# Optimization experiments

Hardware: AMD Instinct MI355X
Metric: run time of the kernel (lower is better)

## Reference

```python
import jax, jax.numpy as jnp
import numpy as np

D_MODEL = 2048
NUM_HEADS = 16
HEAD_DIM = D_MODEL // NUM_HEADS
BATCH = 2
SEQ = 2048


def setup_inputs() -> dict:
    key = jax.random.key(0)
    ks = jax.random.split(key, 5)
    s = 1.0 / np.sqrt(D_MODEL)
    return {
        "x": jax.random.normal(ks[0], (BATCH, SEQ, D_MODEL), dtype=jnp.float32),
        "Wq": jax.random.normal(ks[1], (D_MODEL, D_MODEL), dtype=jnp.float32) * s,
        "Wk": jax.random.normal(ks[2], (D_MODEL, D_MODEL), dtype=jnp.float32) * s,
        "Wv": jax.random.normal(ks[3], (D_MODEL, D_MODEL), dtype=jnp.float32) * s,
        "Wo": jax.random.normal(ks[4], (D_MODEL, D_MODEL), dtype=jnp.float32) * s,
    }


def reference(x, Wq, Wk, Wv, Wo):
    B, S, D = x.shape
    H, Dh = NUM_HEADS, HEAD_DIM
    # nn.Linear(bias=False): y = x @ W.T ; split_heads is a plain view (no transpose!)
    Q = (x @ Wq.T).reshape(B, H, S, Dh)
    K = (x @ Wk.T).reshape(B, H, S, Dh)
    V = (x @ Wv.T).reshape(B, H, S, Dh)
    # scores scaled by head_dim (NOT sqrt) — faithful to source
    scores = jnp.einsum("bhqd,bhkd->bhqk", Q, K) / jnp.float32(Dh)
    causal_mask = jnp.triu(jnp.ones((S, S), dtype=bool), k=1)  # True above diagonal
    scores = jnp.where(causal_mask, -jnp.inf, scores)
    attn = jax.nn.softmax(scores, axis=-1)
    out = jnp.einsum("bhqk,bhkd->bhqd", attn, V)  # [B,H,S,Dh]
    out = out.transpose(0, 2, 1, 3).reshape(B, S, D)  # merge DOES transpose
    return out @ Wo.T
```

## Files before the change

### kernel.cpp

```cpp
#include <hip/hip_runtime.h>
#include <hip/hip_bf16.h>

using bf16 = __hip_bfloat16;
typedef __attribute__((ext_vector_type(8))) short bf16x8;
typedef __attribute__((ext_vector_type(4))) float f32x4;

#define DEVI __device__ __forceinline__

constexpr int Bn = 2, Sn = 2048, Dn = 2048, Hn = 16, DHn = 128;
constexpr int Mn = Bn * Sn;

DEVI void gload_lds16(const bf16* g, bf16* l) {
  __builtin_amdgcn_global_load_lds(
      (__attribute__((address_space(1))) void*)g,
      (__attribute__((address_space(3))) void*)l,
      16, 0, 0);
}

__global__ __launch_bounds__(256) void cvt_all_k(const float* __restrict__ x,
                                                 const float* __restrict__ wq,
                                                 const float* __restrict__ wk,
                                                 const float* __restrict__ wv,
                                                 const float* __restrict__ wo,
                                                 bf16* __restrict__ xb,
                                                 bf16* __restrict__ wb) {
  const int which = blockIdx.y;
  const float* src;
  bf16* dst;
  int n8;
  if (which == 0) { src = x;  dst = xb; n8 = Mn * Dn / 8; }
  else {
    src = (which == 1) ? wq : (which == 2) ? wk : (which == 3) ? wv : wo;
    dst = wb + (size_t)(which - 1) * Dn * Dn;
    n8 = Dn * Dn / 8;
  }
  for (int i = blockIdx.x * 256 + threadIdx.x; i < n8; i += gridDim.x * 256) {
    const float4* p = (const float4*)src + (size_t)i * 2;
    float4 a = p[0], b = p[1];
    union { bf16 h[8]; bf16x8 v; } u;
    u.h[0] = __float2bfloat16(a.x); u.h[1] = __float2bfloat16(a.y);
    u.h[2] = __float2bfloat16(a.z); u.h[3] = __float2bfloat16(a.w);
    u.h[4] = __float2bfloat16(b.x); u.h[5] = __float2bfloat16(b.y);
    u.h[6] = __float2bfloat16(b.z); u.h[7] = __float2bfloat16(b.w);
    *((bf16x8*)dst + i) = u.v;
  }
}

template <int NTOT, int NMAT>
__global__ __launch_bounds__(256, 2) void gemmY(const bf16* __restrict__ A,
                                                const bf16* __restrict__ W,
                                                bf16* __restrict__ Cv) {
  constexpr int K = 2048, NT = 64;
  __shared__ bf16 smem[2 * 12288];

  const int nwg = NTOT * 16;
  const int orig = blockIdx.x;
  const int wgid = (orig & 7) * (nwg >> 3) + (orig >> 3);
  const int bm = wgid / NTOT;
  const int bnn = wgid % NTOT;
  constexpr int nper = NTOT / NMAT;
  const int z = bnn / nper;
  const int col0 = (bnn % nper) * 128;

  const int t = threadIdx.x;
  const int wave = t >> 6, lane = t & 63;
  const int wm = wave >> 1, wn = wave & 1;
  const int lr = lane & 15, lg = lane >> 4;
  const int rch = ((lg ^ ((lr >> 1) & 3)) * 8);
  const int srow = t >> 2;
  const int sch = (t & 3) ^ ((t >> 3) & 3);

  const bf16* Ab = A + (size_t)(bm * 256 + srow) * K + sch * 8;
  const bf16* Bb = W + (size_t)z * (2048 * 2048) +
                   (size_t)(col0 + srow) * K + sch * 8;

  auto stgA = [&](int slot, int kt, int u) {
    gload_lds16(Ab + (size_t)u * 64 * K + kt * 32,
                smem + slot * 12288 + u * 2048 + t * 8);
  };
  auto stgB = [&](int slot, int kt, int v) {
    gload_lds16(Bb + (size_t)v * 64 * K + kt * 32,
                smem + slot * 12288 + 8192 + v * 2048 + t * 8);
  };

  f32x4 acc[8][4];
  const f32x4 zf = {0.f, 0.f, 0.f, 0.f};
#pragma unroll
  for (int i = 0; i < 8; ++i)
#pragma unroll
    for (int j = 0; j < 4; ++j) acc[i][j] = zf;

  stgA(0, 0, 0); stgA(0, 0, 1); stgA(0, 0, 2); stgA(0, 0, 3);
  stgB(0, 0, 0); stgB(0, 0, 1);
  stgA(1, 1, 0); stgA(1, 1, 2); stgB(1, 1, 0); stgB(1, 1, 1);

#pragma unroll 2
  for (int kt = 0; kt < NT; ++kt) {
    const int slot = kt & 1;
    const bf16* sAb = smem + slot * 12288;
    const bf16* sBb = sAb + 8192;

    if (kt == NT - 1) asm volatile("s_waitcnt vmcnt(0)" ::: "memory");
    else              asm volatile("s_waitcnt vmcnt(4)" ::: "memory");
    __builtin_amdgcn_s_barrier();

    bf16x8 af[4], bv[4];
#pragma unroll
    for (int i = 0; i < 4; ++i)
      af[i] = *(const bf16x8*)(sAb + (wm * 128 + i * 16 + lr) * 32 + rch);
#pragma unroll
    for (int n = 0; n < 4; ++n)
      bv[n] = *(const bf16x8*)(sBb + (wn * 64 + n * 16 + lr) * 32 + rch);
    if (kt + 1 < NT) { stgA(slot ^ 1, kt + 1, 1); stgA(slot ^ 1, kt + 1, 3); }
    asm volatile("s_waitcnt lgkmcnt(0)" ::: "memory");
    __builtin_amdgcn_sched_barrier(0);
    __builtin_amdgcn_s_setprio(1);
#pragma unroll
    for (int i = 0; i < 4; ++i)
#pragma unroll
      for (int n = 0; n < 4; ++n)
        acc[i][n] = __builtin_amdgcn_mfma_f32_16x16x32_bf16(af[i], bv[n], acc[i][n], 0, 0, 0);
    __builtin_amdgcn_s_setprio(0);
    __builtin_amdgcn_s_barrier();

#pragma unroll
    for (int i = 0; i < 4; ++i)
      af[i] = *(const bf16x8*)(sAb + (wm * 128 + 64 + i * 16 + lr) * 32 + rch);
    if (kt + 2 < NT) {
      stgA(slot, kt + 2, 0); stgA(slot, kt + 2, 2);
      stgB(slot, kt + 2, 0); stgB(slot, kt + 2, 1);
    }
    asm volatile("s_waitcnt lgkmcnt(0)" ::: "memory");
    __builtin_amdgcn_sched_barrier(0);
    __builtin_amdgcn_s_setprio(1);
#pragma unroll
    for (int i = 0; i < 4; ++i)
#pragma unroll
      for (int n = 0; n < 4; ++n)
        acc[4 + i][n] = __builtin_amdgcn_mfma_f32_16x16x32_bf16(af[i], bv[n], acc[4 + i][n], 0, 0, 0);
    __builtin_amdgcn_s_setprio(0);
  }

  const int r0 = bm * 256 + wm * 128, c0 = col0 + wn * 64;
#pragma unroll
  for (int mm = 0; mm < 8; ++mm)
#pragma unroll
    for (int nn = 0; nn < 4; ++nn) {
      const int rr = r0 + mm * 16 + lg * 4;
      const int cc = c0 + nn * 16 + lr;
      bf16* C = Cv + (size_t)z * (Mn * 2048);
#pragma unroll
      for (int r = 0; r < 4; ++r)
        C[(size_t)(rr + r) * 2048 + cc] = __float2bfloat16(acc[mm][nn][r]);
    }
}

template <int NCT>
__global__ __launch_bounds__(512, 1) void gemm8f(const bf16* __restrict__ A,
                                                 const bf16* __restrict__ W,
                                                 float* __restrict__ Cv) {
  constexpr int K = 2048, NT = K / 64;
  constexpr int SLOTE = (128 + 256) * 64;
  __shared__ bf16 smem[3 * SLOTE];

  constexpr int MT = Mn / 128;
  const int nwg = MT * NCT;
  const int orig = blockIdx.x;
  const int wgid = (orig & 7) * (nwg >> 3) + (orig >> 3);
  const int bm = wgid / NCT;
  const int bcn = wgid % NCT;
  const int col0 = bcn * 256;

  const int t = threadIdx.x;
  const int wave = t >> 6, lane = t & 63;
  const int wm = wave >> 2, wn = wave & 3;
  const int lr = lane & 15, lg = lane >> 4;
  const int swz = lr & 7;

  const int srow = t >> 3;
  const int schk = (t & 7) ^ (srow & 7);
  const bf16* Ab = A + (size_t)(bm * 128 + srow) * K + schk * 8;
  const bf16* Bb = W + (size_t)(col0 + srow) * K + schk * 8;

  auto stgA = [&](int slot, int kt, int u) {
    gload_lds16(Ab + (size_t)u * 64 * K + kt * 64,
                smem + slot * SLOTE + u * 4096 + t * 8);
  };
  auto stgB = [&](int slot, int kt, int u) {
    gload_lds16(Bb + (size_t)u * 64 * K + kt * 64,
                smem + slot * SLOTE + 8192 + u * 4096 + t * 8);
  };

  f32x4 acc[4][4];
  const f32x4 zf = {0.f, 0.f, 0.f, 0.f};
#pragma unroll
  for (int i = 0; i < 4; ++i)
#pragma unroll
    for (int j = 0; j < 4; ++j) acc[i][j] = zf;

  stgA(0, 0, 0); stgA(0, 0, 1);
  stgB(0, 0, 0); stgB(0, 0, 1); stgB(0, 0, 2); stgB(0, 0, 3);
  stgA(1, 1, 0); stgA(1, 1, 1);
  stgB(1, 1, 0); stgB(1, 1, 1); stgB(1, 1, 2); stgB(1, 1, 3);

  int sl = 0;
#pragma unroll 1
  for (int kt = 0; kt < NT; ++kt) {
    const bf16* sA = smem + sl * SLOTE;
    const bf16* sB = sA + 8192;
    int sl2 = sl + 2; if (sl2 >= 3) sl2 -= 3;
    const bool pf = (kt + 2 < NT);

    if (kt == NT - 1) asm volatile("s_waitcnt vmcnt(0)" ::: "memory");
    else              asm volatile("s_waitcnt vmcnt(6)" ::: "memory");
    __builtin_amdgcn_s_barrier();

    {
      bf16x8 af[4], bv[4];
#pragma unroll
      for (int i = 0; i < 4; ++i)
        af[i] = *(const bf16x8*)(sA + (wm * 64 + i * 16 + lr) * 64 + ((lg ^ swz) * 8));
#pragma unroll
      for (int n = 0; n < 4; ++n)
        bv[n] = *(const bf16x8*)(sB + (wn * 64 + n * 16 + lr) * 64 + ((lg ^ swz) * 8));
      if (pf) { stgA(sl2, kt + 2, 0); stgA(sl2, kt + 2, 1); stgB(sl2, kt + 2, 0); }
      __builtin_amdgcn_s_barrier();
      asm volatile("s_waitcnt lgkmcnt(0)" ::: "memory");
      __builtin_amdgcn_sched_barrier(0);
      __builtin_amdgcn_s_setprio(1);
#pragma unroll
      for (int i = 0; i < 4; ++i)
#pragma unroll
        for (int n = 0; n < 4; ++n)
          acc[i][n] = __builtin_amdgcn_mfma_f32_16x16x32_bf16(af[i], bv[n], acc[i][n], 0, 0, 0);
      __builtin_amdgcn_s_setprio(0);
      __builtin_amdgcn_s_barrier();
    }
    {
      bf16x8 af[4], bv[4];
#pragma unroll
      for (int i = 0; i < 4; ++i)
        af[i] = *(const bf16x8*)(sA + (wm * 64 + i * 16 + lr) * 64 + (((4 + lg) ^ swz) * 8));
#pragma unroll
      for (int n = 0; n < 4; ++n)
        bv[n] = *(const bf16x8*)(sB + (wn * 64 + n * 16 + lr) * 64 + (((4 + lg) ^ swz) * 8));
      if (pf) { stgB(sl2, kt + 2, 1); stgB(sl2, kt + 2, 2); stgB(sl2, kt + 2, 3); }
      __builtin_amdgcn_s_barrier();
      asm volatile("s_waitcnt lgkmcnt(0)" ::: "memory");
      __builtin_amdgcn_sched_barrier(0);
      __builtin_amdgcn_s_setprio(1);
#pragma unroll
      for (int i = 0; i < 4; ++i)
#pragma unroll
        for (int n = 0; n < 4; ++n)
          acc[i][n] = __builtin_amdgcn_mfma_f32_16x16x32_bf16(af[i], bv[n], acc[i][n], 0, 0, 0);
      __builtin_amdgcn_s_setprio(0);
    }
    sl = (sl == 2) ? 0 : sl + 1;
  }

  const int r0 = bm * 128 + wm * 64, c0 = col0 + wn * 64;
#pragma unroll
  for (int mm = 0; mm < 4; ++mm)
#pragma unroll
    for (int nn = 0; nn < 4; ++nn) {
      const int rr = r0 + mm * 16 + lg * 4;
      const int cc = c0 + nn * 16 + lr;
#pragma unroll
      for (int r = 0; r < 4; ++r)
        Cv[(size_t)(rr + r) * 2048 + cc] = acc[mm][nn][r];
    }
}

__global__ __launch_bounds__(256, 2) void transpose_v(const bf16* __restrict__ V,
                                                      bf16* __restrict__ VT) {
  __shared__ bf16 tile[128 * 128];
  const int kt = blockIdx.x, bh = blockIdx.y;
  const bf16* Vh = V + (size_t)bh * (Sn * DHn);
  bf16* VTh = VT + (size_t)bh * (DHn * Sn);
  const int t = threadIdx.x;
  const int rr = t >> 4, cc = t & 15;
#pragma unroll
  for (int i = 0; i < 8; ++i) {
    int r = rr + i * 16;
    int ch = cc ^ ((r >> 3) & 7);
    *(bf16x8*)(tile + r * 128 + ch * 8) =
        *(const bf16x8*)(Vh + (size_t)(kt * 128 + r) * DHn + cc * 8);
  }
  __syncthreads();
  const int dr = t >> 4, li = t & 15;
#pragma unroll
  for (int i = 0; i < 8; ++i) {
    int dh = dr + i * 16;
    union { bf16 h[8]; bf16x8 v; } u;
#pragma unroll
    for (int j = 0; j < 8; ++j) {
      int k = li * 8 + j;
      int ch = (dh >> 3) ^ ((k >> 3) & 7);
      u.h[j] = tile[k * 128 + ch * 8 + (dh & 7)];
    }
    *(bf16x8*)(VTh + (size_t)dh * Sn + kt * 128 + li * 8) = u.v;
  }
}

__global__ __launch_bounds__(512, 1) void attn_k5(const bf16* __restrict__ Q,
                                                  const bf16* __restrict__ K,
                                                  const bf16* __restrict__ VT,
                                                  bf16* __restrict__ Mg) {
  __shared__ bf16 smem[57344];
  bf16* sP = smem + 49152;
  bf16* sO = smem;

  const int bi = blockIdx.x;
  const int xcd = bi & 7, slt = bi >> 3;
  const int bh = (slt & 3) * 8 + xcd;
  const int j = slt >> 2;
  const bf16* Qh = Q + (size_t)bh * (Sn * DHn);
  const bf16* Kh = K + (size_t)bh * (Sn * DHn);
  const bf16* VTh = VT + (size_t)bh * (DHn * Sn);
  const int b = bh >> 4, h = bh & 15;

  const int t = threadIdx.x, wave = t >> 6, lane = t & 63;
  const int lr = lane & 15, lg = lane >> 4;

  auto STAGE = [&](int s, int kt) {
    bf16* dK = smem + s * 16384;
    bf16* dV = dK + 8192;
#pragma unroll
    for (int i = 0; i < 2; ++i) {
      int c = i * 512 + t;
      int row = c >> 4, c16 = c & 15;
      gload_lds16(Kh + (size_t)(kt * 64 + row) * DHn + ((c16 ^ (row & 7)) * 8),
                  dK + c * 8);
    }
#pragma unroll
    for (int i = 0; i < 2; ++i) {
      int c = i * 512 + t;
      int row = c >> 3, c8 = c & 7;
      gload_lds16(VTh + (size_t)row * Sn + kt * 64 + ((c8 ^ (row & 7)) * 8),
                  dV + c * 8);
    }
  };

  const f32x4 zf = {0.f, 0.f, 0.f, 0.f};

  for (int pi = 0; pi < 2; ++pi) {
    const int qb = pi ? (15 - j) : j;
    const int nt = qb * 2 + 2;
    const int q0 = qb * 128 + wave * 16;
    const int qg = q0 + lr;

    bf16x8 qf[4];
#pragma unroll
    for (int kk = 0; kk < 4; ++kk)
      qf[kk] = *(const bf16x8*)(Qh + (size_t)(q0 + lr) * DHn + kk * 32 + lg * 8);

    f32x4 o[8];
#pragma unroll
    for (int d = 0; d < 8; ++d) o[d] = zf;
    float mrun = -3e38f, lrun = 0.f;

    STAGE(0, 0);
    STAGE(1, 1);
    asm volatile("s_waitcnt vmcnt(4)" ::: "memory");
    __builtin_amdgcn_s_barrier();

    for (int kt = 0; kt < nt; ++kt) {
      const int sl = kt % 3;
      if (kt + 2 < nt) STAGE((kt + 2) % 3, kt + 2);

      bf16* sKc = smem + sl * 16384;
      bf16* sVc = sKc + 8192;

      f32x4 sfr[4];
#pragma unroll
      for (int nn = 0; nn < 4; ++nn) sfr[nn] = zf;
#pragma unroll
      for (int kk = 0; kk < 4; ++kk)
#pragma unroll
        for (int nn = 0; nn < 4; ++nn) {
          int row = nn * 16 + lr;
          int ch = (kk * 4 + lg) ^ (row & 7);
          bf16x8 kf = *(const bf16x8*)(sKc + row * DHn + ch * 8);
          sfr[nn] = __builtin_amdgcn_mfma_f32_16x16x32_bf16(kf, qf[kk], sfr[nn], 0, 0, 0);
        }

      const bool maskt = (kt >= qb * 2);
      float pv[4][4];
#pragma unroll
      for (int nn = 0; nn < 4; ++nn)
#pragma unroll
        for (int r = 0; r < 4; ++r) {
          float v = sfr[nn][r] * (1.0f / 128.0f);
          if (maskt) {
            int kg = kt * 64 + nn * 16 + lg * 4 + r;
            if (kg > qg) v = -1e30f;
          }
          pv[nn][r] = v;
        }
      float rm = -3e38f;
#pragma unroll
      for (int nn = 0; nn < 4; ++nn)
        rm = fmaxf(rm, fmaxf(fmaxf(pv[nn][0], pv[nn][1]), fmaxf(pv[nn][2], pv[nn][3])));
      rm = fmaxf(rm, __shfl_xor(rm, 16));
      rm = fmaxf(rm, __shfl_xor(rm, 32));
      const float mnew = fmaxf(mrun, rm);
      const float alpha = __expf(mrun - mnew);
      float rsum = 0.f;
#pragma unroll
      for (int nn = 0; nn < 4; ++nn)
#pragma unroll
        for (int r = 0; r < 4; ++r) {
          float p = __expf(pv[nn][r] - mnew);
          pv[nn][r] = p;
          rsum += p;
        }
      rsum += __shfl_xor(rsum, 16);
      rsum += __shfl_xor(rsum, 32);
      lrun = lrun * alpha + rsum;
      const bool grew = (mnew > mrun);
      mrun = mnew;
      if (__any(grew)) {
#pragma unroll
        for (int d = 0; d < 8; ++d)
#pragma unroll
          for (int r = 0; r < 4; ++r) o[d][r] *= alpha;
      }

#pragma unroll
      for (int nn = 0; nn < 4; ++nn)
#pragma unroll
        for (int r = 0; r < 4; ++r) {
          int c = nn * 2 + (lg >> 1);
          int chk = c ^ (lr & 7);
          sP[wave * 1024 + lr * 64 + chk * 8 + (lg & 1) * 4 + r] =
              __float2bfloat16(pv[nn][r]);
        }

      bf16x8 pf[2];
#pragma unroll
      for (int kk = 0; kk < 2; ++kk) {
        int ch = (kk * 4 + lg) ^ (lr & 7);
        pf[kk] = *(const bf16x8*)(sP + wave * 1024 + lr * 64 + ch * 8);
      }
#pragma unroll
      for (int d = 0; d < 8; ++d)
#pragma unroll
        for (int kk = 0; kk < 2; ++kk) {
          int vrow = d * 16 + lr;
          int vch = (kk * 4 + lg) ^ (vrow & 7);
          bf16x8 vf = *(const bf16x8*)(sVc + vrow * 64 + vch * 8);
          o[d] = __builtin_amdgcn_mfma_f32_16x16x32_bf16(vf, pf[kk], o[d], 0, 0, 0);
        }

      if (kt + 2 < nt) asm volatile("s_waitcnt vmcnt(4)" ::: "memory");
      else             asm volatile("s_waitcnt vmcnt(0)" ::: "memory");
      __builtin_amdgcn_s_barrier();
    }

    const float inv = 1.0f / lrun;
#pragma unroll
    for (int d = 0; d < 8; ++d)
#pragma unroll
      for (int r = 0; r < 4; ++r) {
        int row = wave * 16 + lr;
        int col = d * 16 + lg * 4 + r;
        int chk = (col >> 3) ^ (lr & 7);
        sO[row * 128 + chk * 8 + (col & 7)] = __float2bfloat16(o[d][r] * inv);
      }
    __syncthreads();
    bf16* Mh = Mg + ((size_t)(b * Sn + qb * 128)) * Dn + h * DHn;
#pragma unroll
    for (int i = 0; i < 4; ++i) {
      int row = (t >> 4) + i * 32;
      int c16 = t & 15;
      *(bf16x8*)(Mh + (size_t)row * Dn + c16 * 8) =
          *(const bf16x8*)(sO + row * 128 + ((c16 ^ (row & 7)) * 8));
    }
    __syncthreads();
  }
}

extern "C" void kernel_launch(void* const* d_in, const int* in_sizes, int n_in,
                              void* d_out, int out_size, void* d_ws, size_t ws_size,
                              hipStream_t stream) {
  const float* x = (const float*)d_in[0];
  const float* Wq = (const float*)d_in[1];
  const float* Wk = (const float*)d_in[2];
  const float* Wv = (const float*)d_in[3];
  const float* Wo = (const float*)d_in[4];
  float* out = (float*)d_out;

  char* ws = (char*)d_ws;
  bf16* xb = (bf16*)ws;            ws += (size_t)Mn * Dn * 2;
  bf16* Wb = (bf16*)ws;            ws += (size_t)4 * Dn * Dn * 2;
  bf16* QKV = (bf16*)ws;           ws += (size_t)3 * Mn * Dn * 2;
  bf16* VT = (bf16*)ws;            ws += (size_t)Bn * Hn * DHn * Sn * 2;
  bf16* Mg = (bf16*)ws;            ws += (size_t)Mn * Dn * 2;

  cvt_all_k<<<dim3(2048, 5), 256, 0, stream>>>(x, Wq, Wk, Wv, Wo, xb, Wb);

  gemmY<48, 3><<<768, 256, 0, stream>>>(xb, Wb, QKV);

  transpose_v<<<dim3(16, 32), 256, 0, stream>>>(QKV + 2 * (size_t)Mn * Dn, VT);

  attn_k5<<<256, 512, 0, stream>>>(QKV, QKV + (size_t)Mn * Dn, VT, Mg);

  gemm8f<8><<<256, 512, 0, stream>>>(Mg, Wb + 3 * (size_t)Dn * Dn, out);
}
```

Measured before the change: 234.4 us.

## Use 128-wide KV tiles with double buffering in attention kernel

The attention kernel now processes 128 keys per iteration instead of 64 and switches from a three-stage to a two-stage LDS ring, which halves the number of loop iterations and barriers. The causal mask is applied only on the diagonal tile. P is written to LDS and consumed in two halves so the existing P buffer can be reused. The trade-offs are a larger LDS footprint, more live registers for the score fragments, and less prefetch depth, since the loop now waits on all outstanding loads each iteration.

```diff
diff --git a/kernel.cpp b/kernel.cpp
--- a/kernel.cpp
+++ b/kernel.cpp
@@ -303,12 +303,12 @@
   }
 }
 
-__global__ __launch_bounds__(512, 1) void attn_k5(const bf16* __restrict__ Q,
+__global__ __launch_bounds__(512, 1) void attn_k6(const bf16* __restrict__ Q,
                                                   const bf16* __restrict__ K,
                                                   const bf16* __restrict__ VT,
                                                   bf16* __restrict__ Mg) {
-  __shared__ bf16 smem[57344];
-  bf16* sP = smem + 49152;
+  __shared__ bf16 smem[73728];
+  bf16* sP = smem + 65536;
   bf16* sO = smem;
 
   const int bi = blockIdx.x;
@@ -324,20 +324,20 @@
   const int lr = lane & 15, lg = lane >> 4;
 
   auto STAGE = [&](int s, int kt) {
-    bf16* dK = smem + s * 16384;
-    bf16* dV = dK + 8192;
-#pragma unroll
-    for (int i = 0; i < 2; ++i) {
+    bf16* dK = smem + s * 32768;
+    bf16* dV = dK + 16384;
+#pragma unroll
+    for (int i = 0; i < 4; ++i) {
       int c = i * 512 + t;
       int row = c >> 4, c16 = c & 15;
-      gload_lds16(Kh + (size_t)(kt * 64 + row) * DHn + ((c16 ^ (row & 7)) * 8),
+      gload_lds16(Kh + (size_t)(kt * 128 + row) * DHn + ((c16 ^ (row & 7)) * 8),
                   dK + c * 8);
     }
 #pragma unroll
-    for (int i = 0; i < 2; ++i) {
+    for (int i = 0; i < 4; ++i) {
       int c = i * 512 + t;
-      int row = c >> 3, c8 = c & 7;
-      gload_lds16(VTh + (size_t)row * Sn + kt * 64 + ((c8 ^ (row & 7)) * 8),
+      int row = c >> 4, c16 = c & 15;
+      gload_lds16(VTh + (size_t)row * Sn + kt * 128 + ((c16 ^ (row & 7)) * 8),
                   dV + c * 8);
     }
   };
@@ -346,7 +346,7 @@
 
   for (int pi = 0; pi < 2; ++pi) {
     const int qb = pi ? (15 - j) : j;
-    const int nt = qb * 2 + 2;
+    const int nt = qb + 1;
     const int q0 = qb * 128 + wave * 16;
     const int qg = q0 + lr;
 
@@ -361,46 +361,45 @@
     float mrun = -3e38f, lrun = 0.f;
 
     STAGE(0, 0);
-    STAGE(1, 1);
-    asm volatile("s_waitcnt vmcnt(4)" ::: "memory");
+    asm volatile("s_waitcnt vmcnt(0)" ::: "memory");
     __builtin_amdgcn_s_barrier();
 
     for (int kt = 0; kt < nt; ++kt) {
-      const int sl = kt % 3;
-      if (kt + 2 < nt) STAGE((kt + 2) % 3, kt + 2);
-
-      bf16* sKc = smem + sl * 16384;
-      bf16* sVc = sKc + 8192;
-
-      f32x4 sfr[4];
-#pragma unroll
-      for (int nn = 0; nn < 4; ++nn) sfr[nn] = zf;
+      const int sl = kt & 1;
+      if (kt + 1 < nt) STAGE(sl ^ 1, kt + 1);
+
+      bf16* sKc = smem + sl * 32768;
+      bf16* sVc = sKc + 16384;
+
+      f32x4 sfr[8];
+#pragma unroll
+      for (int nn = 0; nn < 8; ++nn) sfr[nn] = zf;
 #pragma unroll
       for (int kk = 0; kk < 4; ++kk)
 #pragma unroll
-        for (int nn = 0; nn < 4; ++nn) {
+        for (int nn = 0; nn < 8; ++nn) {
           int row = nn * 16 + lr;
           int ch = (kk * 4 + lg) ^ (row & 7);
-          bf16x8 kf = *(const bf16x8*)(sKc + row * DHn + ch * 8);
+          bf16x8 kf = *(const bf16x8*)(sKc + row * 128 + ch * 8);
           sfr[nn] = __builtin_amdgcn_mfma_f32_16x16x32_bf16(kf, qf[kk], sfr[nn], 0, 0, 0);
         }
 
-      const bool maskt = (kt >= qb * 2);
-      float pv[4][4];
-#pragma unroll
-      for (int nn = 0; nn < 4; ++nn)
+      const bool maskt = (kt == qb);
+      float pv[8][4];
+#pragma unroll
+      for (int nn = 0; nn < 8; ++nn)
 #pragma unroll
         for (int r = 0; r < 4; ++r) {
           float v = sfr[nn][r] * (1.0f / 128.0f);
           if (maskt) {
-            int kg = kt * 64 + nn * 16 + lg * 4 + r;
+            int kg = kt * 128 + nn * 16 + lg * 4 + r;
             if (kg > qg) v = -1e30f;
           }
           pv[nn][r] = v;
         }
       float rm = -3e38f;
 #pragma unroll
-      for (int nn = 0; nn < 4; ++nn)
+      for (int nn = 0; nn < 8; ++nn)
         rm = fmaxf(rm, fmaxf(fmaxf(pv[nn][0], pv[nn][1]), fmaxf(pv[nn][2], pv[nn][3])));
       rm = fmaxf(rm, __shfl_xor(rm, 16));
       rm = fmaxf(rm, __shfl_xor(rm, 32));
@@ -408,7 +407,7 @@
       const float alpha = __expf(mrun - mnew);
       float rsum = 0.f;
 #pragma unroll
-      for (int nn = 0; nn < 4; ++nn)
+      for (int nn = 0; nn < 8; ++nn)
 #pragma unroll
         for (int r = 0; r < 4; ++r) {
           float p = __expf(pv[nn][r] - mnew);
@@ -428,33 +427,38 @@
       }
 
 #pragma unroll
-      for (int nn = 0; nn < 4; ++nn)
-#pragma unroll
-        for (int r = 0; r < 4; ++r) {
-          int c = nn * 2 + (lg >> 1);
-          int chk = c ^ (lr & 7);
-          sP[wave * 1024 + lr * 64 + chk * 8 + (lg & 1) * 4 + r] =
-              __float2bfloat16(pv[nn][r]);
+      for (int kh = 0; kh < 2; ++kh) {
+        if (kh == 1) {
+          asm volatile("s_waitcnt lgkmcnt(0)" ::: "memory");
+          __builtin_amdgcn_sched_barrier(0);
         }
-
-      bf16x8 pf[2];
-#pragma unroll
-      for (int kk = 0; kk < 2; ++kk) {
-        int ch = (kk * 4 + lg) ^ (lr & 7);
-        pf[kk] = *(const bf16x8*)(sP + wave * 1024 + lr * 64 + ch * 8);
+#pragma unroll
+        for (int nn = 0; nn < 4; ++nn)
+#pragma unroll
+          for (int r = 0; r < 4; ++r) {
+            int c = nn * 2 + (lg >> 1);
+            int chk = c ^ (lr & 7);
+            sP[wave * 1024 + lr * 64 + chk * 8 + (lg & 1) * 4 + r] =
+                __float2bfloat16(pv[kh * 4 + nn][r]);
+          }
+        bf16x8 pf[2];
+#pragma unroll
+        for (int kk = 0; kk < 2; ++kk) {
+          int ch = (kk * 4 + lg) ^ (lr & 7);
+          pf[kk] = *(const bf16x8*)(sP + wave * 1024 + lr * 64 + ch * 8);
+        }
+#pragma unroll
+        for (int d = 0; d < 8; ++d)
+#pragma unroll
+          for (int kk = 0; kk < 2; ++kk) {
+            int vrow = d * 16 + lr;
+            int vch = (kh * 8 + kk * 4 + lg) ^ (vrow & 7);
+            bf16x8 vf = *(const bf16x8*)(sVc + vrow * 128 + vch * 8);
+            o[d] = __builtin_amdgcn_mfma_f32_16x16x32_bf16(vf, pf[kk], o[d], 0, 0, 0);
+          }
       }
-#pragma unroll
-      for (int d = 0; d < 8; ++d)
-#pragma unroll
-        for (int kk = 0; kk < 2; ++kk) {
-          int vrow = d * 16 + lr;
-          int vch = (kk * 4 + lg) ^ (vrow & 7);
-          bf16x8 vf = *(const bf16x8*)(sVc + vrow * 64 + vch * 8);
-          o[d] = __builtin_amdgcn_mfma_f32_16x16x32_bf16(vf, pf[kk], o[d], 0, 0, 0);
-        }
-
-      if (kt + 2 < nt) asm volatile("s_waitcnt vmcnt(4)" ::: "memory");
-      else             asm volatile("s_waitcnt vmcnt(0)" ::: "memory");
+
+      asm volatile("s_waitcnt vmcnt(0)" ::: "memory");
       __builtin_amdgcn_s_barrier();
     }
 
@@ -504,7 +508,7 @@
 
   transpose_v<<<dim3(16, 32), 256, 0, stream>>>(QKV + 2 * (size_t)Mn * Dn, VT);
 
-  attn_k5<<<256, 512, 0, stream>>>(QKV, QKV + (size_t)Mn * Dn, VT, Mg);
+  attn_k6<<<256, 512, 0, stream>>>(QKV, QKV + (size_t)Mn * Dn, VT, Mg);
 
   gemm8f<8><<<256, 512, 0, stream>>>(Mg, Wb + 3 * (size_t)Dn * Dn, out);
 }
```

Result: faster. 227.3 us (-3.0%).
